# Optimization experiments

Hardware: AMD Instinct MI355X
Metric: run time of the kernel (lower is better)

The kernel has to match this reference:

```python
import jax, jax.numpy as jnp
import numpy as np

EMBED_DIM = 1024
NUM_HEADS = 16
HEAD_DIM = EMBED_DIM // NUM_HEADS
MASKED = True


def setup_inputs() -> dict:
    key = jax.random.key(0)
    ks = jax.random.split(key, 9)
    B, S, E = 4, 2048, EMBED_DIM
    sc = 1.0 / np.sqrt(E)
    return {
        "x": jax.random.normal(ks[0], (B, S, E), jnp.float32),
        "wq": jax.random.normal(ks[1], (E, E), jnp.float32) * sc,
        "bq": jax.random.normal(ks[2], (E,), jnp.float32) * 0.02,
        "wk": jax.random.normal(ks[3], (E, E), jnp.float32) * sc,
        "bk": jax.random.normal(ks[4], (E,), jnp.float32) * 0.02,
        "wv": jax.random.normal(ks[5], (E, E), jnp.float32) * sc,
        "bv": jax.random.normal(ks[6], (E,), jnp.float32) * 0.02,
        "wo": jax.random.normal(ks[7], (E, E), jnp.float32) * sc,
        "bo": jax.random.normal(ks[8], (E,), jnp.float32) * 0.02,
    }


def reference(x, wq, bq, wk, bk, wv, bv, wo, bo):
    B, S, E = x.shape
    H, Dh = NUM_HEADS, HEAD_DIM
    # QKV projections, then split heads: [B,S,E] -> [B,H,S,Dh]
    def split(t):
        return t.reshape(B, S, H, Dh).transpose(0, 2, 1, 3)
    q = split(x @ wq.T + bq)
    k = split(x @ wk.T + bk)
    v = split(x @ wv.T + bv)
    scale = Dh ** 0.5
    scores = jnp.einsum('bhsd,bhtd->bhst', q, k) / scale  # [B,H,S,S]
    if MASKED:
        causal = jnp.tril(jnp.ones((S, S), dtype=bool))
        scores = jnp.where(causal, scores, -jnp.inf)
    weights = jax.nn.softmax(scores, axis=-1)
    ctx = jnp.einsum('bhst,bhtd->bhsd', weights, v)
    ctx = ctx.transpose(0, 2, 1, 3).reshape(B, S, E)
    return ctx @ wo.T + bo
```

## Files before the change

kernel.cpp:

```cpp
#include <hip/hip_runtime.h>
#include <hip/hip_bf16.h>

#define EMB   1024
#define SEQ   2048
#define BATCH 4
#define NH    16
#define DHEAD 64
#define MROWS (BATCH*SEQ)
#define NSTRIP (SEQ/32)
#define QSCALE 0.18033688011112042f

typedef float f32x4  __attribute__((ext_vector_type(4)));
typedef float f32x16 __attribute__((ext_vector_type(16)));
typedef short s16x8  __attribute__((ext_vector_type(8)));

__device__ __forceinline__ f32x4 mfma16(s16x8 a, s16x8 b, f32x4 c) {
    return __builtin_amdgcn_mfma_f32_16x16x32_bf16(a, b, c, 0, 0, 0);
}
__device__ __forceinline__ f32x16 mfma32(s16x8 a, s16x8 b, f32x16 c) {
    return __builtin_amdgcn_mfma_f32_32x32x16_bf16(a, b, c, 0, 0, 0);
}

__device__ __forceinline__ unsigned short f2bf(float f) {
    __hip_bfloat16 h = __float2bfloat16(f);
    return __builtin_bit_cast(unsigned short, h);
}

__device__ __forceinline__ unsigned cvtpk(float lo, float hi) {
    unsigned r;
    asm("v_cvt_pk_bf16_f32 %0, %1, %2" : "=v"(r) : "v"(lo), "v"(hi));
    return r;
}

__device__ __forceinline__ void plane_swap(unsigned &a, unsigned &b) {
    asm("v_permlane32_swap_b32 %0, %1" : "+v"(a), "+v"(b));
}

__device__ __forceinline__ s16x8 frag4(unsigned a, unsigned b, unsigned c, unsigned d) {
    union { unsigned u[4]; s16x8 f; } x;
    x.u[0] = a; x.u[1] = b; x.u[2] = c; x.u[3] = d;
    return x.f;
}

__device__ __forceinline__ float exp2r(float x) {
    float r;
    asm("v_exp_f32 %0, %1" : "=v"(r) : "v"(x));
    return r;
}
__device__ __forceinline__ float max3f(float a, float b, float c) {
    float r;
    asm("v_max3_f32 %0, %1, %2, %3" : "=v"(r) : "v"(a), "v"(b), "v"(c));
    return r;
}

__global__ void cvt_bf16(const float* __restrict__ in, unsigned short* __restrict__ out, int n4) {
    int i = blockIdx.x * blockDim.x + threadIdx.x;
    if (i >= n4) return;
    float4 v = reinterpret_cast<const float4*>(in)[i];
    ushort4 o;
    o.x = f2bf(v.x); o.y = f2bf(v.y); o.z = f2bf(v.z); o.w = f2bf(v.w);
    reinterpret_cast<ushort4*>(out)[i] = o;
}

__global__ void cvt_bf16_w(const float* __restrict__ w0, const float* __restrict__ w1,
                           const float* __restrict__ w2, const float* __restrict__ w3,
                           unsigned short* __restrict__ o0, unsigned short* __restrict__ o1,
                           unsigned short* __restrict__ o2, unsigned short* __restrict__ o3,
                           int n4) {
    int i = blockIdx.x * blockDim.x + threadIdx.x;
    if (i >= n4) return;
    const float* in; unsigned short* out;
    switch (blockIdx.y) {
        case 0:  in = w0; out = o0; break;
        case 1:  in = w1; out = o1; break;
        case 2:  in = w2; out = o2; break;
        default: in = w3; out = o3; break;
    }
    float4 v = reinterpret_cast<const float4*>(in)[i];
    ushort4 o;
    o.x = f2bf(v.x); o.y = f2bf(v.y); o.z = f2bf(v.z); o.w = f2bf(v.w);
    reinterpret_cast<ushort4*>(out)[i] = o;
}

#define GLDS(g, s) __builtin_amdgcn_global_load_lds((const __attribute__((address_space(1))) void*)(g), \
                       (__attribute__((address_space(3))) void*)(s), 16, 0, 0)

__global__ __launch_bounds__(256) void gemm_qkv(const unsigned short* __restrict__ A,
                                                const unsigned short* __restrict__ wqb,
                                                const unsigned short* __restrict__ wkb,
                                                const unsigned short* __restrict__ wvb,
                                                const float* __restrict__ bq,
                                                const float* __restrict__ bk,
                                                const float* __restrict__ bv,
                                                unsigned short* __restrict__ qB,
                                                unsigned short* __restrict__ kB,
                                                unsigned short* __restrict__ vtB) {
    __shared__ unsigned short sA0[128*32];
    __shared__ unsigned short sB0[128*32];
    __shared__ unsigned short sA1[128*32];
    __shared__ unsigned short sB1[128*32];
    const int tid = threadIdx.x;
    const int w  = tid >> 6, l = tid & 63;
    const int lg = l >> 4,  lr = l & 15;
    const int nb  = blockIdx.x;
    const int seg = nb >> 3;
    const int mBase = blockIdx.y * 128;
    const int nBase = (nb & 7) * 128;
    const unsigned short* Bw = (seg == 0) ? wqb : (seg == 1) ? wkb : wvb;
    const float* bias = (seg == 0) ? bq : (seg == 1) ? bk : bv;
    const int wr = w >> 1, wc = w & 1;
    const int srow = l >> 2;
    const int sk0  = (l & 3) * 8;
    const bool segV = (seg == 2);

    f32x4 acc[4][4] = {};

    auto STAGE = [&](unsigned short* dA, unsigned short* dB, int kb) {
        #pragma unroll
        for (int rr = 0; rr < 2; ++rr) {
            const int chunk = w + rr * 4;
            const unsigned short* ga = A  + (size_t)(mBase + chunk*16 + srow) * EMB + kb + sk0;
            GLDS(ga, &dA[chunk * 512]);
            const unsigned short* gb = Bw + (size_t)(nBase + chunk*16 + srow) * EMB + kb + sk0;
            GLDS(gb, &dB[chunk * 512]);
        }
    };
    auto COMPUTE = [&](const unsigned short* dA, const unsigned short* dB) {
        s16x8 af[4], bf[4];
        #pragma unroll
        for (int mi = 0; mi < 4; ++mi)
            af[mi] = *reinterpret_cast<const s16x8*>(&dA[(wr*64 + mi*16 + lr)*32 + lg*8]);
        #pragma unroll
        for (int ni = 0; ni < 4; ++ni)
            bf[ni] = *reinterpret_cast<const s16x8*>(&dB[(wc*64 + ni*16 + lr)*32 + lg*8]);
        if (segV) {
            #pragma unroll
            for (int mi = 0; mi < 4; ++mi)
                #pragma unroll
                for (int ni = 0; ni < 4; ++ni)
                    acc[ni][mi] = mfma16(bf[ni], af[mi], acc[ni][mi]);
        } else {
            #pragma unroll
            for (int mi = 0; mi < 4; ++mi)
                #pragma unroll
                for (int ni = 0; ni < 4; ++ni)
                    acc[mi][ni] = mfma16(af[mi], bf[ni], acc[mi][ni]);
        }
    };

    STAGE(sA0, sB0, 0);
    __syncthreads();
    for (int kb = 0; kb < EMB; kb += 64) {
        STAGE(sA1, sB1, kb + 32);
        COMPUTE(sA0, sB0);
        __syncthreads();
        if (kb + 64 < EMB) STAGE(sA0, sB0, kb + 64);
        COMPUTE(sA1, sB1);
        __syncthreads();
    }

    const int colBase = nBase + wc * 64;
    const int rowBase = mBase + wr * 64;
    if (!segV) {
        unsigned short* outp = seg ? kB : qB;
        const float oscale = seg ? 1.0f : QSCALE;
        #pragma unroll
        for (int ni = 0; ni < 4; ++ni) {
            const int col = colBase + ni*16 + lr;
            const float bv = bias[col];
            const int h = col >> 6, d = col & 63;
            const int inner = ((d >> 4) * 2 + ((d >> 3) & 1)) * 256 + (d & 7);
            #pragma unroll
            for (int mi = 0; mi < 4; ++mi) {
                #pragma unroll
                for (int r = 0; r < 4; ++r) {
                    const int gr = rowBase + mi*16 + lg*4 + r;
                    const int b = gr >> 11, sin_ = gr & 2047;
                    const int strip = sin_ >> 5, l31q = sin_ & 31;
                    outp[(size_t)(b*NH + h) * (SEQ*DHEAD) + strip*2048 + inner + l31q*8]
                        = f2bf((acc[mi][ni][r] + bv) * oscale);
                }
            }
        }
    } else {
        unsigned short* outp = vtB;
        #pragma unroll
        for (int ni = 0; ni < 4; ++ni) {
            #pragma unroll
            for (int r = 0; r < 4; ++r) {
                const int n = colBase + ni*16 + lg*4 + r;
                const float bv = bias[n];
                const int h = n >> 6, d = n & 63;
                #pragma unroll
                for (int mi = 0; mi < 4; ++mi) {
                    const int tok = rowBase + mi*16 + lr;
                    const int b = tok >> 11, sv = tok & 2047;
                    const int kvt = sv >> 5, ks = (sv >> 4) & 1, hi2 = (sv >> 3) & 1, j = sv & 7;
                    outp[(size_t)(b*NH + h) * (SEQ*DHEAD) + kvt*2048 + (ks*2 + hi2)*512 + d*8 + j]
                        = f2bf(acc[ni][mi][r] + bv);
                }
            }
        }
    }
}

__global__ __launch_bounds__(256) void gemm_out(const unsigned short* __restrict__ A,
                                                const unsigned short* __restrict__ Bw,
                                                const float* __restrict__ bias,
                                                float* __restrict__ Out) {
    __shared__ unsigned short sA0[128*32];
    __shared__ unsigned short sB0[128*32];
    __shared__ unsigned short sA1[128*32];
    __shared__ unsigned short sB1[128*32];
    const int tid = threadIdx.x;
    const int w  = tid >> 6, l = tid & 63;
    const int lg = l >> 4,  lr = l & 15;
    const int mBase = blockIdx.y * 128;
    const int nBase = blockIdx.x * 128;
    const int wr = w >> 1, wc = w & 1;
    const int srow = l >> 2;
    const int sk0  = (l & 3) * 8;

    f32x4 acc[4][4] = {};

    auto STAGE = [&](unsigned short* dA, unsigned short* dB, int kb) {
        #pragma unroll
        for (int rr = 0; rr < 2; ++rr) {
            const int chunk = w + rr * 4;
            const unsigned short* ga = A  + (size_t)(mBase + chunk*16 + srow) * EMB + kb + sk0;
            GLDS(ga, &dA[chunk * 512]);
            const unsigned short* gb = Bw + (size_t)(nBase + chunk*16 + srow) * EMB + kb + sk0;
            GLDS(gb, &dB[chunk * 512]);
        }
    };
    auto COMPUTE = [&](const unsigned short* dA, const unsigned short* dB) {
        s16x8 af[4], bf[4];
        #pragma unroll
        for (int mi = 0; mi < 4; ++mi)
            af[mi] = *reinterpret_cast<const s16x8*>(&dA[(wr*64 + mi*16 + lr)*32 + lg*8]);
        #pragma unroll
        for (int ni = 0; ni < 4; ++ni)
            bf[ni] = *reinterpret_cast<const s16x8*>(&dB[(wc*64 + ni*16 + lr)*32 + lg*8]);
        #pragma unroll
        for (int mi = 0; mi < 4; ++mi)
            #pragma unroll
            for (int ni = 0; ni < 4; ++ni)
                acc[mi][ni] = mfma16(af[mi], bf[ni], acc[mi][ni]);
    };

    STAGE(sA0, sB0, 0);
    __syncthreads();
    for (int kb = 0; kb < EMB; kb += 64) {
        STAGE(sA1, sB1, kb + 32);
        COMPUTE(sA0, sB0);
        __syncthreads();
        if (kb + 64 < EMB) STAGE(sA0, sB0, kb + 64);
        COMPUTE(sA1, sB1);
        __syncthreads();
    }

    const int colBase = nBase + wc * 64;
    const int rowBase = mBase + wr * 64;
    #pragma unroll
    for (int ni = 0; ni < 4; ++ni) {
        const int col = colBase + ni*16 + lr;
        const float bv = bias[col];
        #pragma unroll
        for (int mi = 0; mi < 4; ++mi) {
            #pragma unroll
            for (int r = 0; r < 4; ++r) {
                const int gr = rowBase + mi*16 + lg*4 + r;
                Out[(size_t)gr * EMB + col] = acc[mi][ni][r] + bv;
            }
        }
    }
}

__global__ __launch_bounds__(64) void attn_fwd(const unsigned short* __restrict__ qb,
                                               const unsigned short* __restrict__ kb,
                                               const unsigned short* __restrict__ vb,
                                               unsigned short* __restrict__ ctx) {
    __shared__ __align__(16) unsigned sld[32*36];
    const int l = threadIdx.x;
    const int l31 = l & 31, hi = l >> 5;
    const int bh = blockIdx.x & 63;
    const int strip = (NSTRIP - 1) - ((int)blockIdx.x >> 6);
    const int q0 = strip * 32;
    const size_t hbase = (size_t)bh * SEQ * DHEAD;
    const unsigned short* qh = qb + hbase;
    const unsigned short* kh = kb + hbase;
    const unsigned short* vh = vb + hbase;

    s16x8 qf[4];
    #pragma unroll
    for (int s = 0; s < 4; ++s)
        qf[s] = *reinterpret_cast<const s16x8*>(&qh[strip*2048 + s*512 + l*8]);

    f32x16 o0 = {}, o1 = {};
    float m = -__builtin_inff(), lsum = 0.f;
    const int ntiles = strip + 1;

    s16x8 kfA[4], vfA[4], kfB[4], vfB[4];

    auto LOADKV = [&](s16x8* kf, s16x8* vf, int t) {
        const unsigned short* kp = kh + t*2048;
        #pragma unroll
        for (int s = 0; s < 4; ++s)
            kf[s] = *reinterpret_cast<const s16x8*>(&kp[s*512 + l*8]);
        const unsigned short* vp = vh + t*2048 + hi*512 + l31*8;
        #pragma unroll
        for (int ks = 0; ks < 2; ++ks) {
            vf[ks]     = *reinterpret_cast<const s16x8*>(&vp[ks*1024]);
            vf[2 + ks] = *reinterpret_cast<const s16x8*>(&vp[ks*1024 + 256]);
        }
    };

    auto BODY = [&](s16x8* kf, s16x8* vf, int t) {
        f32x16 sa = {};
        #pragma unroll
        for (int s = 0; s < 4; ++s) sa = mfma32(kf[s], qf[s], sa);

        if (t == strip) {
            #pragma unroll
            for (int r = 0; r < 16; ++r) {
                const int kvloc = (r & 3) + 8*(r >> 2) + 4*hi;
                if (kvloc > l31) sa[r] = -__builtin_inff();
            }
        }

        const float a0 = max3f(sa[0],  sa[1],  sa[2]);
        const float a1 = max3f(sa[3],  sa[4],  sa[5]);
        const float a2 = max3f(sa[6],  sa[7],  sa[8]);
        const float a3 = max3f(sa[9],  sa[10], sa[11]);
        const float a4 = max3f(sa[12], sa[13], sa[14]);
        const float b0 = max3f(a0, a1, a2);
        const float b1 = max3f(a3, a4, sa[15]);
        float pm = fmaxf(b0, b1);
        pm = fmaxf(pm, __shfl_xor(pm, 32));

        float mn = m;
        if (!__all(pm <= m + 8.0f)) {
            mn = fmaxf(m, pm);
            const float fs = exp2r(m - mn);
            o0 *= fs; o1 *= fs; lsum *= fs;
            m = mn;
        }

        #pragma unroll
        for (int r = 0; r < 16; ++r) sa[r] = exp2r(sa[r] - mn);

        const float s0 = sa[0]+sa[1],   s1 = sa[2]+sa[3],   s2 = sa[4]+sa[5],   s3 = sa[6]+sa[7];
        const float s4 = sa[8]+sa[9],   s5 = sa[10]+sa[11], s6 = sa[12]+sa[13], s7 = sa[14]+sa[15];
        const float t0 = s0+s1, t1 = s2+s3, t2 = s4+s5, t3 = s6+s7;
        float rs = (t0+t1) + (t2+t3);
        rs += __shfl_xor(rs, 32);
        lsum += rs;

        unsigned u[4], v[4];
        #pragma unroll
        for (int r2 = 0; r2 < 4; ++r2) {
            u[r2] = cvtpk(sa[4*r2 + 0], sa[4*r2 + 1]);
            v[r2] = cvtpk(sa[4*r2 + 2], sa[4*r2 + 3]);
        }
        plane_swap(u[0], u[1]); plane_swap(v[0], v[1]);
        plane_swap(u[2], u[3]); plane_swap(v[2], v[3]);
        const s16x8 pf0 = frag4(u[0], v[0], u[1], v[1]);
        const s16x8 pf1 = frag4(u[2], v[2], u[3], v[3]);

        o0 = mfma32(vf[0], pf0, o0);
        o0 = mfma32(vf[1], pf1, o0);
        o1 = mfma32(vf[2], pf0, o1);
        o1 = mfma32(vf[3], pf1, o1);
    };

    LOADKV(kfA, vfA, 0);
    int t = 0;
    for (; t + 1 < ntiles; t += 2) {
        LOADKV(kfB, vfB, t + 1);
        BODY(kfA, vfA, t);
        if (t + 2 < ntiles) LOADKV(kfA, vfA, t + 2);
        BODY(kfB, vfB, t + 1);
    }
    if (t < ntiles) BODY(kfA, vfA, t);

    const float inv = 1.0f / lsum;
    #pragma unroll
    for (int dt = 0; dt < 2; ++dt) {
        #pragma unroll
        for (int r2 = 0; r2 < 4; ++r2) {
            const float e0 = (dt ? o1[4*r2+0] : o0[4*r2+0]) * inv;
            const float e1 = (dt ? o1[4*r2+1] : o0[4*r2+1]) * inv;
            const float e2 = (dt ? o1[4*r2+2] : o0[4*r2+2]) * inv;
            const float e3 = (dt ? o1[4*r2+3] : o0[4*r2+3]) * inv;
            const int col = 4*r2 + 2*hi + 16*dt;
            sld[l31*36 + col]     = cvtpk(e0, e1);
            sld[l31*36 + col + 1] = cvtpk(e2, e3);
        }
    }
    asm volatile("s_waitcnt lgkmcnt(0)" ::: "memory");
    __builtin_amdgcn_sched_barrier(0);
    const int row = l >> 1, half = l & 1;
    const unsigned* rp = &sld[row*36 + half*16];
    const int b = bh >> 4, h = bh & 15;
    unsigned short* op = &ctx[((size_t)b*SEQ + q0 + row) * EMB + h*DHEAD + half*32];
    #pragma unroll
    for (int i = 0; i < 4; ++i) {
        uint4 d4 = *reinterpret_cast<const uint4*>(rp + i*4);
        *reinterpret_cast<uint4*>(op + i*8) = d4;
    }
}

extern "C" void kernel_launch(void* const* d_in, const int* in_sizes, int n_in,
                              void* d_out, int out_size, void* d_ws, size_t ws_size,
                              hipStream_t stream) {
    const float* x  = (const float*)d_in[0];
    const float* wq = (const float*)d_in[1];
    const float* bq = (const float*)d_in[2];
    const float* wk = (const float*)d_in[3];
    const float* bk = (const float*)d_in[4];
    const float* wv = (const float*)d_in[5];
    const float* bv = (const float*)d_in[6];
    const float* wo = (const float*)d_in[7];
    const float* bo = (const float*)d_in[8];
    float* out = (float*)d_out;

    char* ws = (char*)d_ws;
    const size_t MB = 1ull << 20;
    unsigned short* xb  = (unsigned short*)(ws);
    unsigned short* wqb = (unsigned short*)(ws + 16*MB);
    unsigned short* wkb = (unsigned short*)(ws + 18*MB);
    unsigned short* wvb = (unsigned short*)(ws + 20*MB);
    unsigned short* wob = (unsigned short*)(ws + 22*MB);
    unsigned short* qB  = (unsigned short*)(ws + 24*MB);
    unsigned short* kB  = (unsigned short*)(ws + 40*MB);
    unsigned short* vtB = (unsigned short*)(ws + 56*MB);
    unsigned short* ctx = xb;

    const int nx4 = MROWS * EMB / 4;
    const int nw4 = EMB * EMB / 4;
    cvt_bf16<<<(nx4 + 255)/256, 256, 0, stream>>>(x, xb, nx4);
    cvt_bf16_w<<<dim3((nw4 + 255)/256, 4), 256, 0, stream>>>(wq, wk, wv, wo, wqb, wkb, wvb, wob, nw4);

    gemm_qkv<<<dim3(24, MROWS/128), 256, 0, stream>>>(xb, wqb, wkb, wvb, bq, bk, bv, qB, kB, vtB);

    attn_fwd<<<dim3(NSTRIP * BATCH * NH), 64, 0, stream>>>(qB, kB, vtB, ctx);

    gemm_out<<<dim3(EMB/128, MROWS/128), 256, 0, stream>>>(ctx, wob, bo, out);
}
```

Baseline: 183.8 us.

## Pair complementary causal strips per attention block and merge conversion kernels

```diff
diff --git a/kernel.cpp b/kernel.cpp
--- a/kernel.cpp
+++ b/kernel.cpp
@@ -53,29 +53,23 @@
     return r;
 }
 
-__global__ void cvt_bf16(const float* __restrict__ in, unsigned short* __restrict__ out, int n4) {
+__global__ void cvt_all(const float* __restrict__ x,
+                        const float* __restrict__ w0, const float* __restrict__ w1,
+                        const float* __restrict__ w2, const float* __restrict__ w3,
+                        unsigned short* __restrict__ xb,
+                        unsigned short* __restrict__ o0, unsigned short* __restrict__ o1,
+                        unsigned short* __restrict__ o2, unsigned short* __restrict__ o3,
+                        int nx4, int nw4) {
     int i = blockIdx.x * blockDim.x + threadIdx.x;
-    if (i >= n4) return;
-    float4 v = reinterpret_cast<const float4*>(in)[i];
-    ushort4 o;
-    o.x = f2bf(v.x); o.y = f2bf(v.y); o.z = f2bf(v.z); o.w = f2bf(v.w);
-    reinterpret_cast<ushort4*>(out)[i] = o;
-}
-
-__global__ void cvt_bf16_w(const float* __restrict__ w0, const float* __restrict__ w1,
-                           const float* __restrict__ w2, const float* __restrict__ w3,
-                           unsigned short* __restrict__ o0, unsigned short* __restrict__ o1,
-                           unsigned short* __restrict__ o2, unsigned short* __restrict__ o3,
-                           int n4) {
-    int i = blockIdx.x * blockDim.x + threadIdx.x;
-    if (i >= n4) return;
-    const float* in; unsigned short* out;
+    const float* in; unsigned short* out; int n;
     switch (blockIdx.y) {
-        case 0:  in = w0; out = o0; break;
-        case 1:  in = w1; out = o1; break;
-        case 2:  in = w2; out = o2; break;
-        default: in = w3; out = o3; break;
-    }
+        case 0:  in = x;  out = xb; n = nx4; break;
+        case 1:  in = w0; out = o0; n = nw4; break;
+        case 2:  in = w1; out = o1; n = nw4; break;
+        case 3:  in = w2; out = o2; n = nw4; break;
+        default: in = w3; out = o3; n = nw4; break;
+    }
+    if (i >= n) return;
     float4 v = reinterpret_cast<const float4*>(in)[i];
     ushort4 o;
     o.x = f2bf(v.x); o.y = f2bf(v.y); o.z = f2bf(v.z); o.w = f2bf(v.w);
@@ -183,7 +177,6 @@
             }
         }
     } else {
-        unsigned short* outp = vtB;
         #pragma unroll
         for (int ni = 0; ni < 4; ++ni) {
             #pragma unroll
@@ -196,7 +189,7 @@
                     const int tok = rowBase + mi*16 + lr;
                     const int b = tok >> 11, sv = tok & 2047;
                     const int kvt = sv >> 5, ks = (sv >> 4) & 1, hi2 = (sv >> 3) & 1, j = sv & 7;
-                    outp[(size_t)(b*NH + h) * (SEQ*DHEAD) + kvt*2048 + (ks*2 + hi2)*512 + d*8 + j]
+                    vtB[(size_t)(b*NH + h) * (SEQ*DHEAD) + kvt*2048 + (ks*2 + hi2)*512 + d*8 + j]
                         = f2bf(acc[ni][mi][r] + bv);
                 }
             }
@@ -276,15 +269,18 @@
     }
 }
 
-__global__ __launch_bounds__(64) void attn_fwd(const unsigned short* __restrict__ qb,
-                                               const unsigned short* __restrict__ kb,
-                                               const unsigned short* __restrict__ vb,
-                                               unsigned short* __restrict__ ctx) {
-    __shared__ __align__(16) unsigned sld[32*36];
-    const int l = threadIdx.x;
+__global__ __launch_bounds__(128) void attn_fwd(const unsigned short* __restrict__ qb,
+                                                const unsigned short* __restrict__ kb,
+                                                const unsigned short* __restrict__ vb,
+                                                unsigned short* __restrict__ ctx) {
+    __shared__ __align__(16) unsigned sld[2][32*36];
+    const int tid = threadIdx.x;
+    const int wv_ = tid >> 6;
+    const int l = tid & 63;
     const int l31 = l & 31, hi = l >> 5;
     const int bh = blockIdx.x & 63;
-    const int strip = (NSTRIP - 1) - ((int)blockIdx.x >> 6);
+    const int pair = (int)blockIdx.x >> 6;
+    const int strip = wv_ ? (NSTRIP - 1 - pair) : pair;
     const int q0 = strip * 32;
     const size_t hbase = (size_t)bh * SEQ * DHEAD;
     const unsigned short* qh = qb + hbase;
@@ -384,6 +380,7 @@
     if (t < ntiles) BODY(kfA, vfA, t);
 
     const float inv = 1.0f / lsum;
+    unsigned* my = sld[wv_];
     #pragma unroll
     for (int dt = 0; dt < 2; ++dt) {
         #pragma unroll
@@ -393,14 +390,14 @@
             const float e2 = (dt ? o1[4*r2+2] : o0[4*r2+2]) * inv;
             const float e3 = (dt ? o1[4*r2+3] : o0[4*r2+3]) * inv;
             const int col = 4*r2 + 2*hi + 16*dt;
-            sld[l31*36 + col]     = cvtpk(e0, e1);
-            sld[l31*36 + col + 1] = cvtpk(e2, e3);
+            my[l31*36 + col]     = cvtpk(e0, e1);
+            my[l31*36 + col + 1] = cvtpk(e2, e3);
         }
     }
     asm volatile("s_waitcnt lgkmcnt(0)" ::: "memory");
     __builtin_amdgcn_sched_barrier(0);
     const int row = l >> 1, half = l & 1;
-    const unsigned* rp = &sld[row*36 + half*16];
+    const unsigned* rp = &my[row*36 + half*16];
     const int b = bh >> 4, h = bh & 15;
     unsigned short* op = &ctx[((size_t)b*SEQ + q0 + row) * EMB + h*DHEAD + half*32];
     #pragma unroll
@@ -438,12 +435,12 @@
 
     const int nx4 = MROWS * EMB / 4;
     const int nw4 = EMB * EMB / 4;
-    cvt_bf16<<<(nx4 + 255)/256, 256, 0, stream>>>(x, xb, nx4);
-    cvt_bf16_w<<<dim3((nw4 + 255)/256, 4), 256, 0, stream>>>(wq, wk, wv, wo, wqb, wkb, wvb, wob, nw4);
+    cvt_all<<<dim3((nx4 + 255)/256, 5), 256, 0, stream>>>(x, wq, wk, wv, wo,
+                                                          xb, wqb, wkb, wvb, wob, nx4, nw4);
 
     gemm_qkv<<<dim3(24, MROWS/128), 256, 0, stream>>>(xb, wqb, wkb, wvb, bq, bk, bv, qB, kB, vtB);
 
-    attn_fwd<<<dim3(NSTRIP * BATCH * NH), 64, 0, stream>>>(qB, kB, vtB, ctx);
+    attn_fwd<<<dim3((NSTRIP/2) * BATCH * NH), 128, 0, stream>>>(qB, kB, vtB, ctx);
 
     gemm_out<<<dim3(EMB/128, MROWS/128), 256, 0, stream>>>(ctx, wob, bo, out);
 }
```

Result: slower. 191.9 us (+4.4%).
